# Kernel tuning notes

Hardware: AMD Instinct MI355X
Metric: run time of the kernel (lower is better)

Reference implementation:

```python
import jax, jax.numpy as jnp
import numpy as np

MIN_ROUGHNESS = 0.08
MAX_ROUGHNESS = 0.5
N_MIPS = 6  # 512 -> 16 cubemap mip chain


def _safe_normalize(x, eps=1e-20):
    return x * jax.lax.rsqrt(jnp.clip(jnp.sum(x * x, -1, keepdims=True), eps, None))


def _dot(a, b):
    return jnp.sum(a * b, -1, keepdims=True)


def _cube_face_uv(d):
    # nvdiffrast cube addressing (matches util.cube_to_dir face layout)
    x, y, z = d[..., 0], d[..., 1], d[..., 2]
    ax, ay, az = jnp.abs(x), jnp.abs(y), jnp.abs(z)
    is_x = (ax >= ay) & (ax >= az)
    is_y = (~is_x) & (ay >= az)
    face = jnp.where(is_x, jnp.where(x >= 0, 0, 1),
           jnp.where(is_y, jnp.where(y >= 0, 2, 3), jnp.where(z >= 0, 4, 5)))
    ma = jnp.maximum(jnp.where(is_x, ax, jnp.where(is_y, ay, az)), 1e-20)
    u = jnp.where(face == 0, -z, jnp.where(face == 1, z, jnp.where(face == 5, -x, x))) / ma
    v = jnp.where(face == 2, z, jnp.where(face == 3, -z, -y)) / ma
    return face, u, v


def _bilinear_cube(tex, face, u, v):
    # tex: [6,R,R,C]; face/u/v: [...]; edge-clamped bilinear within the face
    R = tex.shape[1]
    tu = (u * 0.5 + 0.5) * R - 0.5
    tv = (v * 0.5 + 0.5) * R - 0.5
    x0 = jnp.floor(tu); y0 = jnp.floor(tv)
    fx = (tu - x0)[..., None]; fy = (tv - y0)[..., None]
    x0i = jnp.clip(x0, 0, R - 1).astype(jnp.int32)
    x1i = jnp.clip(x0 + 1, 0, R - 1).astype(jnp.int32)
    y0i = jnp.clip(y0, 0, R - 1).astype(jnp.int32)
    y1i = jnp.clip(y0 + 1, 0, R - 1).astype(jnp.int32)
    c00 = tex[face, y0i, x0i]; c01 = tex[face, y0i, x1i]
    c10 = tex[face, y1i, x0i]; c11 = tex[face, y1i, x1i]
    return (c00 * (1 - fx) + c01 * fx) * (1 - fy) + (c10 * (1 - fx) + c11 * fx) * fy


def _sample_cubemap(tex, dirs):
    f, u, v = _cube_face_uv(dirs)
    return _bilinear_cube(tex, f, u, v)


def _sample_2d_clamp(tex, uv):
    # tex: [H,W,C]; uv in [0,1]^2, clamp boundary bilinear (FG LUT lookup)
    H, W = tex.shape[0], tex.shape[1]
    tu = uv[..., 0] * W - 0.5
    tv = uv[..., 1] * H - 0.5
    x0 = jnp.floor(tu); y0 = jnp.floor(tv)
    fx = (tu - x0)[..., None]; fy = (tv - y0)[..., None]
    x0i = jnp.clip(x0, 0, W - 1).astype(jnp.int32)
    x1i = jnp.clip(x0 + 1, 0, W - 1).astype(jnp.int32)
    y0i = jnp.clip(y0, 0, H - 1).astype(jnp.int32)
    y1i = jnp.clip(y0 + 1, 0, H - 1).astype(jnp.int32)
    c00 = tex[y0i, x0i]; c01 = tex[y0i, x1i]
    c10 = tex[y1i, x0i]; c11 = tex[y1i, x1i]
    return (c00 * (1 - fx) + c01 * fx) * (1 - fy) + (c10 * (1 - fx) + c11 * fx) * fy


def _get_mip(r, n_levels):
    lo = (jnp.clip(r, MIN_ROUGHNESS, MAX_ROUGHNESS) - MIN_ROUGHNESS) / (MAX_ROUGHNESS - MIN_ROUGHNESS) * (n_levels - 2)
    hi = (jnp.clip(r, MAX_ROUGHNESS, 1.0) - MAX_ROUGHNESS) / (1.0 - MAX_ROUGHNESS) + (n_levels - 2)
    return jnp.where(r < MAX_ROUGHNESS, lo, hi)


def _linear2srgb(x):
    xs = jnp.where(x > 0.0031308, x, 1.0)  # avoid pow(0) grad issues
    return jnp.where(x > 0.0031308, 1.055 * jnp.power(xs, 1.0 / 2.4) - 0.055, 12.92 * x)


def _avg_pool_cube(c):
    F, R, _, C = c.shape
    return c.reshape(F, R // 2, 2, R // 2, 2, C).mean(axis=(2, 4))


def setup_inputs() -> dict:
    key = jax.random.key(0)
    ks = jax.random.split(key, 10)
    B, H, W = 1, 1024, 1024
    gb_pos = jax.random.normal(ks[0], (B, H, W, 3), jnp.float32)
    gb_normal = _safe_normalize(jax.random.normal(ks[1], (B, H, W, 3), jnp.float32))
    basecolor = jax.random.uniform(ks[2], (B, H, W, 3), jnp.float32)
    metallic = jax.random.uniform(ks[3], (B, H, W, 1), jnp.float32)
    roughness = jax.random.uniform(ks[4], (B, H, W, 1), jnp.float32)
    view_pos = jax.random.normal(ks[5], (1, 1, 1, 3), jnp.float32) * 3.0
    diffuse = jax.random.uniform(ks[6], (6, 16, 16, 3), jnp.float32)
    fg_lut = jax.random.uniform(ks[7], (256, 256, 2), jnp.float32)
    specs = {}
    s = jax.random.uniform(ks[8], (6, 512, 512, 3), jnp.float32)
    for l in range(N_MIPS):
        specs['spec%d' % l] = s
        if l < N_MIPS - 1:
            s = _avg_pool_cube(s)
    return dict(gb_pos=gb_pos, gb_normal=gb_normal, basecolor=basecolor,
                metallic=metallic, roughness=roughness, view_pos=view_pos,
                diffuse=diffuse, fg_lut=fg_lut, **specs)


def reference(gb_pos, gb_normal, basecolor, metallic, roughness, view_pos,
              diffuse, fg_lut, spec0, spec1, spec2, spec3, spec4, spec5):
    specs = [spec0, spec1, spec2, spec3, spec4, spec5]
    L = len(specs)
    metallic = metallic[..., :1]
    wo = _safe_normalize(view_pos - gb_pos)
    diffuse_albedo = (1.0 - metallic) * basecolor
    specular_albedo = 0.04 * (1.0 - metallic) + metallic * basecolor
    reflvec = _safe_normalize(2.0 * _dot(wo, gb_normal) * gb_normal - wo)
    # diffuse IBL: cubemap gather along normal
    ambient = _sample_cubemap(diffuse, gb_normal)
    diffuse_linear = ambient * diffuse_albedo
    # FG LUT gather
    NdotV = jnp.clip(_dot(wo, gb_normal), 1e-4, None)
    fg = _sample_2d_clamp(fg_lut, jnp.concatenate([NdotV, roughness], -1))
    # trilinear (linear-mipmap-linear) specular cubemap gather
    mip = jnp.clip(_get_mip(roughness[..., 0], L), 0.0, L - 1.0)
    face, u, v = _cube_face_uv(reflvec)
    spec = jnp.zeros(gb_pos.shape[:-1] + (spec0.shape[-1],), gb_pos.dtype)
    for l in range(L):
        w = jnp.clip(1.0 - jnp.abs(mip - l), 0.0, 1.0)[..., None]
        spec = spec + w * _bilinear_cube(specs[l], face, u, v)
    reflectance = specular_albedo * fg[..., 0:1] + fg[..., 1:2]
    rgb = spec * reflectance + diffuse_linear
    return _linear2srgb(jnp.clip(rgb, 0.0, 1.0))
```

## Files before the change

### kernel.cpp

```cpp
#include <hip/hip_runtime.h>
#include <hip/hip_fp16.h>

struct V3 { float x, y, z; };

__device__ __forceinline__ V3 v3add(V3 a, V3 b){ return {a.x+b.x, a.y+b.y, a.z+b.z}; }
__device__ __forceinline__ V3 v3sub(V3 a, V3 b){ return {a.x-b.x, a.y-b.y, a.z-b.z}; }
__device__ __forceinline__ V3 v3scale(V3 a, float s){ return {a.x*s, a.y*s, a.z*s}; }
__device__ __forceinline__ V3 v3mul(V3 a, V3 b){ return {a.x*b.x, a.y*b.y, a.z*b.z}; }
__device__ __forceinline__ float dot3(V3 a, V3 b){ return fmaf(a.x,b.x, fmaf(a.y,b.y, a.z*b.z)); }
__device__ __forceinline__ V3 nrm3(V3 a){
    float s = rsqrtf(fmaxf(dot3(a,a), 1e-20f));
    return v3scale(a, s);
}

#define OFF0 0
#define OFF1 1572864
#define OFF2 1966080
#define OFF3 2064384
#define OFF4 2088960
#define OFF5 2095104
#define DIFF_OFF 2096640
#define SPEC_DIFF_COUNT 2098176

struct __align__(16) PairBlock { __half2 h01, h23, h45, h67; };
#define FG_OFF 2098176
#define TOTAL_BLOCKS 2163712
#define PACK_ONLY_BLOCKS 2098176
#define WS_BYTES_FULL  ((size_t)TOTAL_BLOCKS * 16)
#define WS_BYTES_PACK  ((size_t)PACK_ONLY_BLOCKS * 16)

#define Q10_FG_COUNT 65536
#define Q10_COUNT (SPEC_DIFF_COUNT + Q10_FG_COUNT)
#define APP_DIFF 0
#define APP_M5   1536
#define APP_UINTS 3072
#define WS_BYTES_Q10M ((size_t)Q10_COUNT * 16 + (size_t)APP_UINTS * 4)

__device__ __forceinline__ void cube_face_uv(V3 d, int& face, float& u, float& v){
    float ax = fabsf(d.x), ay = fabsf(d.y), az = fabsf(d.z);
    bool is_x = (ax >= ay) && (ax >= az);
    bool is_y = (!is_x) && (ay >= az);
    face = is_x ? (d.x >= 0.f ? 0 : 1)
                : (is_y ? (d.y >= 0.f ? 2 : 3)
                        : (d.z >= 0.f ? 4 : 5));
    float ma = fmaxf(is_x ? ax : (is_y ? ay : az), 1e-20f);
    float un = (face == 0) ? -d.z : (face == 1) ? d.z : (face == 5) ? -d.x : d.x;
    float vn = (face == 2) ?  d.z : (face == 3) ? -d.z : -d.y;
    float inv = 1.0f / ma;
    u = un * inv;
    v = vn * inv;
}

__device__ __forceinline__ void quad_coord_cube(float u, float v, int R,
                                                int& xq, int& yq, float& fx, float& fy){
    float Rf = (float)R;
    float tu = fmaf(fmaf(u, 0.5f, 0.5f), Rf, -0.5f);
    float tv = fmaf(fmaf(v, 0.5f, 0.5f), Rf, -0.5f);
    float x0f = floorf(tu), y0f = floorf(tv);
    fx = tu - x0f; fy = tv - y0f;
    int x0 = (int)x0f, y0 = (int)y0f;
    fx = (x0 < 0) ? 0.f : fx;
    fy = (y0 < 0) ? 0.f : fy;
    xq = min(max(x0, 0), R-1);
    yq = min(max(y0, 0), R-1);
}

__device__ __forceinline__ void quad_coord_2d(float u, float v, int W, int H,
                                              int& xq, int& yq, float& fx, float& fy){
    float tu = fmaf(u, (float)W, -0.5f);
    float tv = fmaf(v, (float)H, -0.5f);
    float x0f = floorf(tu), y0f = floorf(tv);
    fx = tu - x0f; fy = tv - y0f;
    int x0 = (int)x0f, y0 = (int)y0f;
    fx = (x0 < 0) ? 0.f : fx;
    fy = (y0 < 0) ? 0.f : fy;
    xq = min(max(x0, 0), W-1);
    yq = min(max(y0, 0), H-1);
}

__device__ __forceinline__ V3 q10_blend(uint4 q, float fx, float fy){
    float w00 = (1.f-fx)*(1.f-fy), w01 = fx*(1.f-fy);
    float w10 = (1.f-fx)*fy,       w11 = fx*fy;
    float r = (float)(q.x & 1023u)*w00 + (float)(q.y & 1023u)*w01
            + (float)(q.z & 1023u)*w10 + (float)(q.w & 1023u)*w11;
    float g = (float)((q.x>>10) & 1023u)*w00 + (float)((q.y>>10) & 1023u)*w01
            + (float)((q.z>>10) & 1023u)*w10 + (float)((q.w>>10) & 1023u)*w11;
    float b = (float)((q.x>>20) & 1023u)*w00 + (float)((q.y>>20) & 1023u)*w01
            + (float)((q.z>>20) & 1023u)*w10 + (float)((q.w>>20) & 1023u)*w11;
    const float s = 1.0f/1023.0f;
    return { r*s, g*s, b*s };
}

__device__ __forceinline__ void q10_fg(uint4 q, float fx, float fy,
                                       float& fa, float& fb){
    float w00 = (1.f-fx)*(1.f-fy), w01 = fx*(1.f-fy);
    float w10 = (1.f-fx)*fy,       w11 = fx*fy;
    float a00 = (float)(q.x & 1023u),        b00 = (float)((q.x>>10) & 1023u);
    float a01 = (float)((q.x>>20) & 1023u),  b01 = (float)(q.y & 1023u);
    float a10 = (float)((q.y>>10) & 1023u),  b10 = (float)((q.y>>20) & 1023u);
    float a11 = (float)(q.z & 1023u),        b11 = (float)((q.z>>10) & 1023u);
    const float s = 1.0f/1023.0f;
    fa = (a00*w00 + a01*w01 + a10*w10 + a11*w11) * s;
    fb = (b00*w00 + b01*w01 + b10*w10 + b11*w11) * s;
}

__device__ __forceinline__ V3 lds_bilin(const unsigned* lds, int base, int R,
                                        int face, float u, float v){
    float Rf = (float)R;
    float tu = fmaf(fmaf(u, 0.5f, 0.5f), Rf, -0.5f);
    float tv = fmaf(fmaf(v, 0.5f, 0.5f), Rf, -0.5f);
    float x0f = floorf(tu), y0f = floorf(tv);
    float fx = tu - x0f, fy = tv - y0f;
    int x0 = min(max((int)x0f,     0), R-1);
    int x1 = min(max((int)x0f + 1, 0), R-1);
    int y0 = min(max((int)y0f,     0), R-1);
    int y1 = min(max((int)y0f + 1, 0), R-1);
    const unsigned* fb = lds + base + face * R * R;
    uint4 q = make_uint4(fb[y0*R + x0], fb[y0*R + x1],
                         fb[y1*R + x0], fb[y1*R + x1]);
    return q10_blend(q, fx, fy);
}

__device__ __forceinline__ void pair_extract(const PairBlock& pb, V3& lo, V3& hi){
    lo.x = __low2float(pb.h01);  lo.y = __high2float(pb.h01); lo.z = __low2float(pb.h23);
    hi.x = __high2float(pb.h23); hi.y = __low2float(pb.h45);  hi.z = __high2float(pb.h45);
}

__device__ __forceinline__ V3 bilinear_pairtex(const PairBlock* __restrict__ lvl, int R,
                                               int face, float u, float v){
    float Rf = (float)R;
    float tu = fmaf(fmaf(u, 0.5f, 0.5f), Rf, -0.5f);
    float tv = fmaf(fmaf(v, 0.5f, 0.5f), Rf, -0.5f);
    float x0f = floorf(tu), y0f = floorf(tv);
    float fx = tu - x0f,    fy = tv - y0f;
    int x0 = (int)x0f;
    fx = (x0 < 0) ? 0.f : fx;
    int xb  = min(max(x0, 0), R-1);
    int y0i = min(max((int)y0f,     0), R-1);
    int y1i = min(max((int)y0f + 1, 0), R-1);
    const PairBlock* fb = lvl + (size_t)face * R * R;
    PairBlock b0 = fb[(size_t)y0i * R + xb];
    PairBlock b1 = fb[(size_t)y1i * R + xb];
    V3 l0, h0, l1, h1;
    pair_extract(b0, l0, h0);
    pair_extract(b1, l1, h1);
    V3 r0 = { l0.x + (h0.x-l0.x)*fx, l0.y + (h0.y-l0.y)*fx, l0.z + (h0.z-l0.z)*fx };
    V3 r1 = { l1.x + (h1.x-l1.x)*fx, l1.y + (h1.y-l1.y)*fx, l1.z + (h1.z-l1.z)*fx };
    return { r0.x + (r1.x-r0.x)*fy, r0.y + (r1.y-r0.y)*fy, r0.z + (r1.z-r0.z)*fy };
}

__device__ __forceinline__ void sample_fg_pair(const float4* __restrict__ fgp,
                                               float u, float v, float& fa, float& fb){
    const int W = 256, H = 256;
    float tu = fmaf(u, (float)W, -0.5f);
    float tv = fmaf(v, (float)H, -0.5f);
    float x0f = floorf(tu), y0f = floorf(tv);
    float fx = tu - x0f,    fy = tv - y0f;
    int x0 = (int)x0f;
    fx = (x0 < 0) ? 0.f : fx;
    int xb  = min(max(x0, 0), W-1);
    int y0i = min(max((int)y0f,     0), H-1);
    int y1i = min(max((int)y0f + 1, 0), H-1);
    float4 r0 = fgp[(size_t)y0i * W + xb];
    float4 r1 = fgp[(size_t)y1i * W + xb];
    float t0a = r0.x + (r0.z - r0.x)*fx, t0b = r0.y + (r0.w - r0.y)*fx;
    float t1a = r1.x + (r1.z - r1.x)*fx, t1b = r1.y + (r1.w - r1.y)*fx;
    fa = t0a + (t1a - t0a)*fy;
    fb = t0b + (t1b - t0b)*fy;
}

__device__ __forceinline__ V3 bilinear_cube3(const float* __restrict__ tex, int R,
                                             int face, float u, float v){
    float Rf = (float)R;
    float tu = fmaf(fmaf(u, 0.5f, 0.5f), Rf, -0.5f);
    float tv = fmaf(fmaf(v, 0.5f, 0.5f), Rf, -0.5f);
    float x0 = floorf(tu), y0 = floorf(tv);
    float fx = tu - x0,    fy = tv - y0;
    int x0i = min(max((int)x0,     0), R-1);
    int x1i = min(max((int)x0 + 1, 0), R-1);
    int y0i = min(max((int)y0,     0), R-1);
    int y1i = min(max((int)y0 + 1, 0), R-1);
    const float* base = tex + (size_t)face * R * R * 3;
    const float* r0 = base + (size_t)y0i * R * 3;
    const float* r1 = base + (size_t)y1i * R * 3;
    float a0 = r0[3*x0i], a1 = r0[3*x0i+1], a2 = r0[3*x0i+2];
    float b0 = r0[3*x1i], b1 = r0[3*x1i+1], b2 = r0[3*x1i+2];
    float d0 = r1[3*x0i], d1 = r1[3*x0i+1], d2 = r1[3*x0i+2];
    float e0 = r1[3*x1i], e1 = r1[3*x1i+1], e2 = r1[3*x1i+2];
    float w00 = (1.f-fx)*(1.f-fy), w01 = fx*(1.f-fy);
    float w10 = (1.f-fx)*fy,       w11 = fx*fy;
    V3 out;
    out.x = a0*w00 + b0*w01 + d0*w10 + e0*w11;
    out.y = a1*w00 + b1*w01 + d1*w10 + e1*w11;
    out.z = a2*w00 + b2*w01 + d2*w10 + e2*w11;
    return out;
}

__device__ __forceinline__ void sample_fg(const float* __restrict__ lut,
                                          float u, float v, float& fa, float& fb){
    const int W = 256, H = 256;
    float tu = fmaf(u, (float)W, -0.5f);
    float tv = fmaf(v, (float)H, -0.5f);
    float x0 = floorf(tu), y0 = floorf(tv);
    float fx = tu - x0,    fy = tv - y0;
    int x0i = min(max((int)x0,     0), W-1);
    int x1i = min(max((int)x0 + 1, 0), W-1);
    int y0i = min(max((int)y0,     0), H-1);
    int y1i = min(max((int)y0 + 1, 0), H-1);
    const float2* l2 = (const float2*)lut;
    float2 a = l2[(size_t)y0i*W + x0i];
    float2 b = l2[(size_t)y0i*W + x1i];
    float2 d = l2[(size_t)y1i*W + x0i];
    float2 e = l2[(size_t)y1i*W + x1i];
    float w00 = (1.f-fx)*(1.f-fy), w01 = fx*(1.f-fy);
    float w10 = (1.f-fx)*fy,       w11 = fx*fy;
    fa = a.x*w00 + b.x*w01 + d.x*w10 + e.x*w11;
    fb = a.y*w00 + b.y*w01 + d.y*w10 + e.y*w11;
}

__device__ __forceinline__ float lin2srgb(float x){
    float xs = (x > 0.0031308f) ? x : 1.0f;
    float p  = __builtin_amdgcn_exp2f(__builtin_amdgcn_logf(xs) * (1.0f/2.4f));
    return (x > 0.0031308f) ? fmaf(1.055f, p, -0.055f) : 12.92f * x;
}

__device__ __forceinline__ float clamp01(float x){ return fminf(fmaxf(x, 0.f), 1.f); }

struct PixPre {
    V3 diff_alb, spec_alb;
    int sface; float su, sv;
    int dface; float du, dv;
    int offA, RA, offB, RB; float f;
    float ndotv, rough;
};

__device__ __forceinline__ PixPre pre_pixel(
    int i,
    const float* __restrict__ gb_pos, const float* __restrict__ gb_normal,
    const float* __restrict__ basecolor, const float* __restrict__ metallic,
    const float* __restrict__ roughness, V3 vp)
{
    V3 pos = { gb_pos[3*i],    gb_pos[3*i+1],    gb_pos[3*i+2] };
    V3 nrm = { gb_normal[3*i], gb_normal[3*i+1], gb_normal[3*i+2] };
    V3 bc  = { basecolor[3*i], basecolor[3*i+1], basecolor[3*i+2] };
    float m = metallic[i];
    float r = roughness[i];

    V3 wo = nrm3(v3sub(vp, pos));
    float ndv_raw = dot3(wo, nrm);
    V3 refl = nrm3(v3sub(v3scale(nrm, 2.0f*ndv_raw), wo));

    PixPre p;
    float one_m = 1.0f - m;
    p.diff_alb = v3scale(bc, one_m);
    p.spec_alb = { fmaf(m, bc.x, 0.04f*one_m),
                   fmaf(m, bc.y, 0.04f*one_m),
                   fmaf(m, bc.z, 0.04f*one_m) };
    p.ndotv = fmaxf(ndv_raw, 0.0001f);
    p.rough = r;

    const float MIN_R = 0.08f, MAX_R = 0.5f;
    float lo = (fminf(fmaxf(r, MIN_R), MAX_R) - MIN_R) / (MAX_R - MIN_R) * 4.0f;
    float hi = (fminf(fmaxf(r, MAX_R), 1.0f) - MAX_R) / (1.0f - MAX_R) + 4.0f;
    float mip = (r < MAX_R) ? lo : hi;
    mip = fminf(fmaxf(mip, 0.0f), 5.0f);
    int l0 = min((int)mip, 5);
    p.f = mip - (float)l0;
    int l1 = min(l0 + 1, 5);

    int offA = OFF0;
    offA = (l0 == 1) ? OFF1 : offA; offA = (l0 == 2) ? OFF2 : offA;
    offA = (l0 == 3) ? OFF3 : offA; offA = (l0 == 4) ? OFF4 : offA;
    offA = (l0 == 5) ? OFF5 : offA;
    int offB = OFF0;
    offB = (l1 == 1) ? OFF1 : offB; offB = (l1 == 2) ? OFF2 : offB;
    offB = (l1 == 3) ? OFF3 : offB; offB = (l1 == 4) ? OFF4 : offB;
    offB = (l1 == 5) ? OFF5 : offB;
    p.offA = offA; p.RA = 512 >> l0;
    p.offB = offB; p.RB = 512 >> l1;

    cube_face_uv(nrm, p.dface, p.du, p.dv);
    cube_face_uv(refl, p.sface, p.su, p.sv);
    return p;
}

__device__ __forceinline__ unsigned pk3(float a, float b, float c){
    unsigned ia = __float2uint_rn(fminf(fmaxf(a, 0.f), 1.f) * 1023.f);
    unsigned ib = __float2uint_rn(fminf(fmaxf(b, 0.f), 1.f) * 1023.f);
    unsigned ic = __float2uint_rn(fminf(fmaxf(c, 0.f), 1.f) * 1023.f);
    return ia | (ib << 10) | (ic << 20);
}

__global__ __launch_bounds__(256)
void pack_q10m_kernel(const float* __restrict__ s0, const float* __restrict__ s1,
                      const float* __restrict__ s2, const float* __restrict__ s3,
                      const float* __restrict__ s4, const float* __restrict__ s5,
                      const float* __restrict__ diffuse, const float* __restrict__ fg_lut,
                      uint4* __restrict__ qws)
{
    int t = blockIdx.x * blockDim.x + threadIdx.x;
    if (t >= Q10_COUNT + APP_UINTS) return;
    if (t >= Q10_COUNT) {
        int local = t - Q10_COUNT;
        const float* src; int idx;
        if (local < APP_M5) { src = diffuse; idx = local; }
        else                { src = s5;      idx = local - APP_M5; }
        ((unsigned*)(qws + Q10_COUNT))[local] = pk3(src[3*idx], src[3*idx+1], src[3*idx+2]);
        return;
    }
    if (t >= SPEC_DIFF_COUNT) {
        int local = t - SPEC_DIFF_COUNT;
        int x = local & 255, y = local >> 8;
        int i00 = local;
        int i01 = (x == 255) ? local : local + 1;
        int i10 = (y == 255) ? local : local + 256;
        int i11 = (x == 255) ? i10 : i10 + 1;
        uint4 q;
        q.x = pk3(fg_lut[2*i00], fg_lut[2*i00+1], fg_lut[2*i01]);
        q.y = pk3(fg_lut[2*i01+1], fg_lut[2*i10], fg_lut[2*i10+1]);
        q.z = pk3(fg_lut[2*i11], fg_lut[2*i11+1], 0.f);
        q.w = 0u;
        qws[t] = q;
        return;
    }
    const float* src; int local; int Rm, Rsh;
    if      (t >= DIFF_OFF) { src = diffuse; local = t - DIFF_OFF; Rm = 15;  Rsh = 4; }
    else if (t >= OFF5)     { src = s5;      local = t - OFF5;     Rm = 15;  Rsh = 4; }
    else if (t >= OFF4)     { src = s4;      local = t - OFF4;     Rm = 31;  Rsh = 5; }
    else if (t >= OFF3)     { src = s3;      local = t - OFF3;     Rm = 63;  Rsh = 6; }
    else if (t >= OFF2)     { src = s2;      local = t - OFF2;     Rm = 127; Rsh = 7; }
    else if (t >= OFF1)     { src = s1;      local = t - OFF1;     Rm = 255; Rsh = 8; }
    else                    { src = s0;      local = t;            Rm = 511; Rsh = 9; }
    int x = local & Rm;
    int y = (local >> Rsh) & Rm;
    int i00 = local;
    int i01 = (x == Rm) ? local : local + 1;
    int i10 = (y == Rm) ? local : local + (Rm + 1);
    int i11 = (x == Rm) ? i10 : i10 + 1;
    uint4 q;
    q.x = pk3(src[3*i00], src[3*i00+1], src[3*i00+2]);
    q.y = pk3(src[3*i01], src[3*i01+1], src[3*i01+2]);
    q.z = pk3(src[3*i10], src[3*i10+1], src[3*i10+2]);
    q.w = pk3(src[3*i11], src[3*i11+1], src[3*i11+2]);
    qws[t] = q;
}

__device__ __forceinline__ V3 sample_spec(const uint4* __restrict__ qws,
                                          const unsigned* lds,
                                          int off, int R, int face, float u, float v){
    if (R == 16)
        return lds_bilin(lds, APP_M5, 16, face, u, v);
    int x, y; float fx, fy;
    quad_coord_cube(u, v, R, x, y, fx, fy);
    size_t q = (size_t)off + (size_t)face * R * R + (size_t)y * R + x;
    return q10_blend(qws[q], fx, fy);
}

__global__ __launch_bounds__(256)
void envlight_q10m(const float* __restrict__ gb_pos,
                   const float* __restrict__ gb_normal,
                   const float* __restrict__ basecolor,
                   const float* __restrict__ metallic,
                   const float* __restrict__ roughness,
                   const float* __restrict__ view_pos,
                   const uint4* __restrict__ qws,
                   float* __restrict__ out,
                   int n)
{
    __shared__ unsigned lds_small[APP_UINTS];
    {
        const uint4* app4 = qws + Q10_COUNT;
        uint4* l4 = (uint4*)lds_small;
        for (int k = threadIdx.x; k < APP_UINTS/4; k += 256)
            l4[k] = app4[k];
    }
    __syncthreads();

    int i = blockIdx.x * blockDim.x + threadIdx.x;
    if (i >= n) return;
    V3 vp = { view_pos[0], view_pos[1], view_pos[2] };
    PixPre p = pre_pixel(i, gb_pos, gb_normal, basecolor, metallic, roughness, vp);

    int fx_, fy_; float ffx, ffy;
    quad_coord_2d(p.ndotv, p.rough, 256, 256, fx_, fy_, ffx, ffy);
    uint4 F = qws[(size_t)SPEC_DIFF_COUNT + (size_t)fy_ * 256 + fx_];

    V3 specA = sample_spec(qws, lds_small, p.offA, p.RA, p.sface, p.su, p.sv);
    V3 specB = sample_spec(qws, lds_small, p.offB, p.RB, p.sface, p.su, p.sv);
    V3 ambient = lds_bilin(lds_small, APP_DIFF, 16, p.dface, p.du, p.dv);

    float fa, fb;
    q10_fg(F, ffx, ffy, fa, fb);

    V3 spec = { specA.x + (specB.x - specA.x) * p.f,
                specA.y + (specB.y - specA.y) * p.f,
                specA.z + (specB.z - specA.z) * p.f };
    V3 reflc = { fmaf(p.spec_alb.x, fa, fb),
                 fmaf(p.spec_alb.y, fa, fb),
                 fmaf(p.spec_alb.z, fa, fb) };
    V3 rgb = v3add(v3mul(spec, reflc), v3mul(ambient, p.diff_alb));

    out[3*i+0] = lin2srgb(clamp01(rgb.x));
    out[3*i+1] = lin2srgb(clamp01(rgb.y));
    out[3*i+2] = lin2srgb(clamp01(rgb.z));
}

__global__ __launch_bounds__(256)
void pack_kernel(const float* __restrict__ s0, const float* __restrict__ s1,
                 const float* __restrict__ s2, const float* __restrict__ s3,
                 const float* __restrict__ s4, const float* __restrict__ s5,
                 const float* __restrict__ diffuse, const float* __restrict__ fg_lut,
                 PairBlock* __restrict__ ws, int total)
{
    int t = blockIdx.x * blockDim.x + threadIdx.x;
    if (t >= total) return;
    if (t >= FG_OFF) {
        int local = t - FG_OFF;
        int x = local & 255;
        int nb = (x == 255) ? local : local + 1;
        float4 v = make_float4(fg_lut[2*local], fg_lut[2*local+1],
                               fg_lut[2*nb],    fg_lut[2*nb+1]);
        ((float4*)ws)[t] = v;
        return;
    }
    const float* src; int local; int Rmask;
    if      (t >= DIFF_OFF) { src = diffuse; local = t - DIFF_OFF; Rmask = 15;  }
    else if (t >= OFF5)     { src = s5;      local = t - OFF5;     Rmask = 15;  }
    else if (t >= OFF4)     { src = s4;      local = t - OFF4;     Rmask = 31;  }
    else if (t >= OFF3)     { src = s3;      local = t - OFF3;     Rmask = 63;  }
    else if (t >= OFF2)     { src = s2;      local = t - OFF2;     Rmask = 127; }
    else if (t >= OFF1)     { src = s1;      local = t - OFF1;     Rmask = 255; }
    else                    { src = s0;      local = t;            Rmask = 511; }
    int nb = ((local & Rmask) == Rmask) ? local : local + 1;
    float ar = src[3*local], ag = src[3*local+1], ab = src[3*local+2];
    float br = src[3*nb],    bg = src[3*nb+1],    bb = src[3*nb+2];
    PairBlock pb;
    pb.h01 = __floats2half2_rn(ar, ag);
    pb.h23 = __floats2half2_rn(ab, br);
    pb.h45 = __floats2half2_rn(bg, bb);
    pb.h67 = __floats2half2_rn(0.f, 0.f);
    ws[t] = pb;
}

template <bool FGPAIR>
__global__ __launch_bounds__(256)
void envlight_pair(const float* __restrict__ gb_pos,
                   const float* __restrict__ gb_normal,
                   const float* __restrict__ basecolor,
                   const float* __restrict__ metallic,
                   const float* __restrict__ roughness,
                   const float* __restrict__ view_pos,
                   const float* __restrict__ fg_lut,
                   const PairBlock* __restrict__ ws,
                   float* __restrict__ out,
                   int n)
{
    int i = blockIdx.x * blockDim.x + threadIdx.x;
    if (i >= n) return;
    V3 vp = { view_pos[0], view_pos[1], view_pos[2] };
    PixPre p = pre_pixel(i, gb_pos, gb_normal, basecolor, metallic, roughness, vp);
    V3 specA   = bilinear_pairtex(ws + p.offA, p.RA, p.sface, p.su, p.sv);
    V3 specB   = bilinear_pairtex(ws + p.offB, p.RB, p.sface, p.su, p.sv);
    V3 ambient = bilinear_pairtex(ws + DIFF_OFF, 16, p.dface, p.du, p.dv);
    float fa, fb;
    if (FGPAIR) sample_fg_pair((const float4*)(ws + FG_OFF), p.ndotv, p.rough, fa, fb);
    else        sample_fg(fg_lut, p.ndotv, p.rough, fa, fb);
    V3 spec = { specA.x + (specB.x - specA.x) * p.f,
                specA.y + (specB.y - specA.y) * p.f,
                specA.z + (specB.z - specA.z) * p.f };
    V3 reflc = { fmaf(p.spec_alb.x, fa, fb),
                 fmaf(p.spec_alb.y, fa, fb),
                 fmaf(p.spec_alb.z, fa, fb) };
    V3 rgb = v3add(v3mul(spec, reflc), v3mul(ambient, p.diff_alb));
    out[3*i+0] = lin2srgb(clamp01(rgb.x));
    out[3*i+1] = lin2srgb(clamp01(rgb.y));
    out[3*i+2] = lin2srgb(clamp01(rgb.z));
}

__global__ __launch_bounds__(256)
void envlight_fallback(const float* __restrict__ gb_pos,
                       const float* __restrict__ gb_normal,
                       const float* __restrict__ basecolor,
                       const float* __restrict__ metallic,
                       const float* __restrict__ roughness,
                       const float* __restrict__ view_pos,
                       const float* __restrict__ diffuse,
                       const float* __restrict__ fg_lut,
                       const float* __restrict__ s0, const float* __restrict__ s1,
                       const float* __restrict__ s2, const float* __restrict__ s3,
                       const float* __restrict__ s4, const float* __restrict__ s5,
                       float* __restrict__ out, int n)
{
    int i = blockIdx.x * blockDim.x + threadIdx.x;
    if (i >= n) return;
    V3 vp = { view_pos[0], view_pos[1], view_pos[2] };
    PixPre p = pre_pixel(i, gb_pos, gb_normal, basecolor, metallic, roughness, vp);
    int l0 = 0;
    l0 = (p.offA == OFF1) ? 1 : l0; l0 = (p.offA == OFF2) ? 2 : l0;
    l0 = (p.offA == OFF3) ? 3 : l0; l0 = (p.offA == OFF4) ? 4 : l0;
    l0 = (p.offA == OFF5) ? 5 : l0;
    int l1 = 0;
    l1 = (p.offB == OFF1) ? 1 : l1; l1 = (p.offB == OFF2) ? 2 : l1;
    l1 = (p.offB == OFF3) ? 3 : l1; l1 = (p.offB == OFF4) ? 4 : l1;
    l1 = (p.offB == OFF5) ? 5 : l1;
    const float* tA = s0;
    tA = (l0 == 1) ? s1 : tA; tA = (l0 == 2) ? s2 : tA;
    tA = (l0 == 3) ? s3 : tA; tA = (l0 == 4) ? s4 : tA; tA = (l0 == 5) ? s5 : tA;
    const float* tB = s0;
    tB = (l1 == 1) ? s1 : tB; tB = (l1 == 2) ? s2 : tB;
    tB = (l1 == 3) ? s3 : tB; tB = (l1 == 4) ? s4 : tB; tB = (l1 == 5) ? s5 : tB;
    V3 ambient = bilinear_cube3(diffuse, 16, p.dface, p.du, p.dv);
    V3 specA   = bilinear_cube3(tA, p.RA, p.sface, p.su, p.sv);
    V3 specB   = bilinear_cube3(tB, p.RB, p.sface, p.su, p.sv);
    float fa, fb;
    sample_fg(fg_lut, p.ndotv, p.rough, fa, fb);
    V3 spec = { specA.x + (specB.x - specA.x) * p.f,
                specA.y + (specB.y - specA.y) * p.f,
                specA.z + (specB.z - specA.z) * p.f };
    V3 reflc = { fmaf(p.spec_alb.x, fa, fb),
                 fmaf(p.spec_alb.y, fa, fb),
                 fmaf(p.spec_alb.z, fa, fb) };
    V3 rgb = v3add(v3mul(spec, reflc), v3mul(ambient, p.diff_alb));
    out[3*i+0] = lin2srgb(clamp01(rgb.x));
    out[3*i+1] = lin2srgb(clamp01(rgb.y));
    out[3*i+2] = lin2srgb(clamp01(rgb.z));
}

extern "C" void kernel_launch(void* const* d_in, const int* in_sizes, int n_in,
                              void* d_out, int out_size, void* d_ws, size_t ws_size,
                              hipStream_t stream) {
    const float* gb_pos    = (const float*)d_in[0];
    const float* gb_normal = (const float*)d_in[1];
    const float* basecolor = (const float*)d_in[2];
    const float* metallic  = (const float*)d_in[3];
    const float* roughness = (const float*)d_in[4];
    const float* view_pos  = (const float*)d_in[5];
    const float* diffuse   = (const float*)d_in[6];
    const float* fg_lut    = (const float*)d_in[7];
    const float* s0        = (const float*)d_in[8];
    const float* s1        = (const float*)d_in[9];
    const float* s2        = (const float*)d_in[10];
    const float* s3        = (const float*)d_in[11];
    const float* s4        = (const float*)d_in[12];
    const float* s5        = (const float*)d_in[13];
    float* out = (float*)d_out;

    int n = in_sizes[0] / 3;
    int block = 256;
    int grid = (n + block - 1) / block;

    if (ws_size >= WS_BYTES_Q10M) {
        uint4* qws = (uint4*)d_ws;
        int ptotal = Q10_COUNT + APP_UINTS;
        int pgrid = (ptotal + block - 1) / block;
        pack_q10m_kernel<<<pgrid, block, 0, stream>>>(s0, s1, s2, s3, s4, s5,
                                                      diffuse, fg_lut, qws);
        envlight_q10m<<<grid, block, 0, stream>>>(gb_pos, gb_normal, basecolor,
            metallic, roughness, view_pos, qws, out, n);
    } else if (ws_size >= WS_BYTES_PACK) {
        bool full = ws_size >= WS_BYTES_FULL;
        PairBlock* ws = (PairBlock*)d_ws;
        int total = full ? TOTAL_BLOCKS : PACK_ONLY_BLOCKS;
        int pgrid = (total + block - 1) / block;
        pack_kernel<<<pgrid, block, 0, stream>>>(s0, s1, s2, s3, s4, s5,
                                                 diffuse, fg_lut, ws, total);
        if (full)
            envlight_pair<true><<<grid, block, 0, stream>>>(gb_pos, gb_normal,
                basecolor, metallic, roughness, view_pos, fg_lut, ws, out, n);
        else
            envlight_pair<false><<<grid, block, 0, stream>>>(gb_pos, gb_normal,
                basecolor, metallic, roughness, view_pos, fg_lut, ws, out, n);
    } else {
        envlight_fallback<<<grid, block, 0, stream>>>(gb_pos, gb_normal, basecolor,
            metallic, roughness, view_pos, diffuse, fg_lut,
            s0, s1, s2, s3, s4, s5, out, n);
    }
}
```

Measured before the change: 152.4 us.

## Vectorize pack and shading kernels to process four texels/pixels per thread

The pack kernel now handles four packed quad-texels per thread, reading source rows with float4 loads and reusing the packed neighbors, so each source value is loaded and quantized once rather than four times. The shading kernel processes four pixels per thread with float4 loads and stores on the AoS inputs and output. This cuts redundant global loads and scalar 4-byte accesses. In exchange there are 4x fewer threads, which lowers occupancy and latency hiding for the gather-heavy shading, and register pressure goes up.

```diff
diff --git a/kernel.cpp b/kernel.cpp
--- a/kernel.cpp
+++ b/kernel.cpp
@@ -35,6 +35,11 @@
 #define APP_M5   1536
 #define APP_UINTS 3072
 #define WS_BYTES_Q10M ((size_t)Q10_COUNT * 16 + (size_t)APP_UINTS * 4)
+
+#define Q4_SPEC (SPEC_DIFF_COUNT/4)
+#define Q4_FG   (Q10_FG_COUNT/4)
+#define Q4_APP  (APP_UINTS/4)
+#define Q4_TOTAL (Q4_SPEC + Q4_FG + Q4_APP)
 
 __device__ __forceinline__ void cube_face_uv(V3 d, int& face, float& u, float& v){
     float ax = fabsf(d.x), ay = fabsf(d.y), az = fabsf(d.z);
@@ -234,18 +239,8 @@
     float ndotv, rough;
 };
 
-__device__ __forceinline__ PixPre pre_pixel(
-    int i,
-    const float* __restrict__ gb_pos, const float* __restrict__ gb_normal,
-    const float* __restrict__ basecolor, const float* __restrict__ metallic,
-    const float* __restrict__ roughness, V3 vp)
-{
-    V3 pos = { gb_pos[3*i],    gb_pos[3*i+1],    gb_pos[3*i+2] };
-    V3 nrm = { gb_normal[3*i], gb_normal[3*i+1], gb_normal[3*i+2] };
-    V3 bc  = { basecolor[3*i], basecolor[3*i+1], basecolor[3*i+2] };
-    float m = metallic[i];
-    float r = roughness[i];
-
+__device__ __forceinline__ PixPre pre_pixel_v(V3 pos, V3 nrm, V3 bc, float m, float r, V3 vp)
+{
     V3 wo = nrm3(v3sub(vp, pos));
     float ndv_raw = dot3(wo, nrm);
     V3 refl = nrm3(v3sub(v3scale(nrm, 2.0f*ndv_raw), wo));
@@ -284,6 +279,18 @@
     return p;
 }
 
+__device__ __forceinline__ PixPre pre_pixel(
+    int i,
+    const float* __restrict__ gb_pos, const float* __restrict__ gb_normal,
+    const float* __restrict__ basecolor, const float* __restrict__ metallic,
+    const float* __restrict__ roughness, V3 vp)
+{
+    V3 pos = { gb_pos[3*i],    gb_pos[3*i+1],    gb_pos[3*i+2] };
+    V3 nrm = { gb_normal[3*i], gb_normal[3*i+1], gb_normal[3*i+2] };
+    V3 bc  = { basecolor[3*i], basecolor[3*i+1], basecolor[3*i+2] };
+    return pre_pixel_v(pos, nrm, bc, metallic[i], roughness[i], vp);
+}
+
 __device__ __forceinline__ unsigned pk3(float a, float b, float c){
     unsigned ia = __float2uint_rn(fminf(fmaxf(a, 0.f), 1.f) * 1023.f);
     unsigned ib = __float2uint_rn(fminf(fmaxf(b, 0.f), 1.f) * 1023.f);
@@ -292,57 +299,100 @@
 }
 
 __global__ __launch_bounds__(256)
-void pack_q10m_kernel(const float* __restrict__ s0, const float* __restrict__ s1,
-                      const float* __restrict__ s2, const float* __restrict__ s3,
-                      const float* __restrict__ s4, const float* __restrict__ s5,
-                      const float* __restrict__ diffuse, const float* __restrict__ fg_lut,
-                      uint4* __restrict__ qws)
+void pack_q10m_v4(const float* __restrict__ s0, const float* __restrict__ s1,
+                  const float* __restrict__ s2, const float* __restrict__ s3,
+                  const float* __restrict__ s4, const float* __restrict__ s5,
+                  const float* __restrict__ diffuse, const float* __restrict__ fg_lut,
+                  uint4* __restrict__ qws)
 {
     int t = blockIdx.x * blockDim.x + threadIdx.x;
-    if (t >= Q10_COUNT + APP_UINTS) return;
-    if (t >= Q10_COUNT) {
-        int local = t - Q10_COUNT;
+    if (t >= Q4_TOTAL) return;
+
+    if (t >= Q4_SPEC + Q4_FG) {
+        int local4 = (t - Q4_SPEC - Q4_FG) * 4;
         const float* src; int idx;
-        if (local < APP_M5) { src = diffuse; idx = local; }
-        else                { src = s5;      idx = local - APP_M5; }
-        ((unsigned*)(qws + Q10_COUNT))[local] = pk3(src[3*idx], src[3*idx+1], src[3*idx+2]);
+        if (local4 < APP_M5) { src = diffuse; idx = local4; }
+        else                 { src = s5;      idx = local4 - APP_M5; }
+        const float4* sp = (const float4*)(src + 3*idx);
+        float4 a = sp[0], b = sp[1], c = sp[2];
+        uint4 o;
+        o.x = pk3(a.x, a.y, a.z);
+        o.y = pk3(a.w, b.x, b.y);
+        o.z = pk3(b.z, b.w, c.x);
+        o.w = pk3(c.y, c.z, c.w);
+        *(uint4*)((unsigned*)(qws + Q10_COUNT) + local4) = o;
         return;
     }
-    if (t >= SPEC_DIFF_COUNT) {
-        int local = t - SPEC_DIFF_COUNT;
+
+    if (t >= Q4_SPEC) {
+        int local = (t - Q4_SPEC) * 4;
         int x = local & 255, y = local >> 8;
-        int i00 = local;
-        int i01 = (x == 255) ? local : local + 1;
-        int i10 = (y == 255) ? local : local + 256;
-        int i11 = (x == 255) ? i10 : i10 + 1;
-        uint4 q;
-        q.x = pk3(fg_lut[2*i00], fg_lut[2*i00+1], fg_lut[2*i01]);
-        q.y = pk3(fg_lut[2*i01+1], fg_lut[2*i10], fg_lut[2*i10+1]);
-        q.z = pk3(fg_lut[2*i11], fg_lut[2*i11+1], 0.f);
-        q.w = 0u;
-        qws[t] = q;
+        int y1 = (y == 255) ? y : y + 1;
+        const float* r0p = fg_lut + 2*local;
+        const float* r1p = fg_lut + 2*((y1 << 8) + x);
+        bool edge = (x == 252);
+        float4 r0a = ((const float4*)r0p)[0], r0b = ((const float4*)r0p)[1];
+        float4 r1a = ((const float4*)r1p)[0], r1b = ((const float4*)r1p)[1];
+        float4 r0c = *(const float4*)(r0p + (edge ? 4 : 8));
+        float4 r1c = *(const float4*)(r1p + (edge ? 4 : 8));
+        float a0[5], b0[5], a1[5], b1[5];
+        a0[0]=r0a.x; b0[0]=r0a.y; a0[1]=r0a.z; b0[1]=r0a.w;
+        a0[2]=r0b.x; b0[2]=r0b.y; a0[3]=r0b.z; b0[3]=r0b.w;
+        a0[4]= edge ? r0b.z : r0c.x; b0[4]= edge ? r0b.w : r0c.y;
+        a1[0]=r1a.x; b1[0]=r1a.y; a1[1]=r1a.z; b1[1]=r1a.w;
+        a1[2]=r1b.x; b1[2]=r1b.y; a1[3]=r1b.z; b1[3]=r1b.w;
+        a1[4]= edge ? r1b.z : r1c.x; b1[4]= edge ? r1b.w : r1c.y;
+        #pragma unroll
+        for (int k = 0; k < 4; ++k) {
+            uint4 q;
+            q.x = pk3(a0[k], b0[k], a0[k+1]);
+            q.y = pk3(b0[k+1], a1[k], b1[k]);
+            q.z = pk3(a1[k+1], b1[k+1], 0.f);
+            q.w = 0u;
+            qws[(size_t)SPEC_DIFF_COUNT + local + k] = q;
+        }
         return;
     }
-    const float* src; int local; int Rm, Rsh;
-    if      (t >= DIFF_OFF) { src = diffuse; local = t - DIFF_OFF; Rm = 15;  Rsh = 4; }
-    else if (t >= OFF5)     { src = s5;      local = t - OFF5;     Rm = 15;  Rsh = 4; }
-    else if (t >= OFF4)     { src = s4;      local = t - OFF4;     Rm = 31;  Rsh = 5; }
-    else if (t >= OFF3)     { src = s3;      local = t - OFF3;     Rm = 63;  Rsh = 6; }
-    else if (t >= OFF2)     { src = s2;      local = t - OFF2;     Rm = 127; Rsh = 7; }
-    else if (t >= OFF1)     { src = s1;      local = t - OFF1;     Rm = 255; Rsh = 8; }
-    else                    { src = s0;      local = t;            Rm = 511; Rsh = 9; }
+
+    int local4q = t * 4;
+    const float* src; int local; int Rm;
+    if      (local4q >= DIFF_OFF) { src = diffuse; local = local4q - DIFF_OFF; Rm = 15;  }
+    else if (local4q >= OFF5)     { src = s5;      local = local4q - OFF5;     Rm = 15;  }
+    else if (local4q >= OFF4)     { src = s4;      local = local4q - OFF4;     Rm = 31;  }
+    else if (local4q >= OFF3)     { src = s3;      local = local4q - OFF3;     Rm = 63;  }
+    else if (local4q >= OFF2)     { src = s2;      local = local4q - OFF2;     Rm = 127; }
+    else if (local4q >= OFF1)     { src = s1;      local = local4q - OFF1;     Rm = 255; }
+    else                          { src = s0;      local = local4q;            Rm = 511; }
     int x = local & Rm;
-    int y = (local >> Rsh) & Rm;
-    int i00 = local;
-    int i01 = (x == Rm) ? local : local + 1;
-    int i10 = (y == Rm) ? local : local + (Rm + 1);
-    int i11 = (x == Rm) ? i10 : i10 + 1;
-    uint4 q;
-    q.x = pk3(src[3*i00], src[3*i00+1], src[3*i00+2]);
-    q.y = pk3(src[3*i01], src[3*i01+1], src[3*i01+2]);
-    q.z = pk3(src[3*i10], src[3*i10+1], src[3*i10+2]);
-    q.w = pk3(src[3*i11], src[3*i11+1], src[3*i11+2]);
-    qws[t] = q;
+    int y = (local / (Rm + 1)) & Rm;
+    int rowUp = (y == Rm) ? 0 : (Rm + 1);
+    const float* r0p = src + 3*local;
+    const float* r1p = src + 3*(local + rowUp);
+    bool edge = (x + 4 > Rm);
+    float4 A0 = ((const float4*)r0p)[0], A1 = ((const float4*)r0p)[1], A2 = ((const float4*)r0p)[2];
+    float4 B0 = ((const float4*)r1p)[0], B1 = ((const float4*)r1p)[1], B2 = ((const float4*)r1p)[2];
+    float4 A3 = *(const float4*)(r0p + (edge ? 8 : 12));
+    float4 B3 = *(const float4*)(r1p + (edge ? 8 : 12));
+    unsigned t0[5], t1[5];
+    t0[0] = pk3(A0.x, A0.y, A0.z);
+    t0[1] = pk3(A0.w, A1.x, A1.y);
+    t0[2] = pk3(A1.z, A1.w, A2.x);
+    t0[3] = pk3(A2.y, A2.z, A2.w);
+    t0[4] = edge ? t0[3] : pk3(A3.x, A3.y, A3.z);
+    t1[0] = pk3(B0.x, B0.y, B0.z);
+    t1[1] = pk3(B0.w, B1.x, B1.y);
+    t1[2] = pk3(B1.z, B1.w, B2.x);
+    t1[3] = pk3(B2.y, B2.z, B2.w);
+    t1[4] = edge ? t1[3] : pk3(B3.x, B3.y, B3.z);
+    #pragma unroll
+    for (int k = 0; k < 4; ++k) {
+        uint4 q;
+        q.x = t0[k];
+        q.y = t0[k+1];
+        q.z = t1[k];
+        q.w = t1[k+1];
+        qws[(size_t)local4q + k] = q;
+    }
 }
 
 __device__ __forceinline__ V3 sample_spec(const uint4* __restrict__ qws,
@@ -356,16 +406,46 @@
     return q10_blend(qws[q], fx, fy);
 }
 
+__device__ __forceinline__ void shade_px(V3 pos, V3 nrm, V3 bc, float m, float r, V3 vp,
+                                         const uint4* __restrict__ qws,
+                                         const unsigned* lds, float* o)
+{
+    PixPre p = pre_pixel_v(pos, nrm, bc, m, r, vp);
+
+    int fx_, fy_; float ffx, ffy;
+    quad_coord_2d(p.ndotv, p.rough, 256, 256, fx_, fy_, ffx, ffy);
+    uint4 F = qws[(size_t)SPEC_DIFF_COUNT + (size_t)fy_ * 256 + fx_];
+
+    V3 specA = sample_spec(qws, lds, p.offA, p.RA, p.sface, p.su, p.sv);
+    V3 specB = sample_spec(qws, lds, p.offB, p.RB, p.sface, p.su, p.sv);
+    V3 ambient = lds_bilin(lds, APP_DIFF, 16, p.dface, p.du, p.dv);
+
+    float fa, fb;
+    q10_fg(F, ffx, ffy, fa, fb);
+
+    V3 spec = { specA.x + (specB.x - specA.x) * p.f,
+                specA.y + (specB.y - specA.y) * p.f,
+                specA.z + (specB.z - specA.z) * p.f };
+    V3 reflc = { fmaf(p.spec_alb.x, fa, fb),
+                 fmaf(p.spec_alb.y, fa, fb),
+                 fmaf(p.spec_alb.z, fa, fb) };
+    V3 rgb = v3add(v3mul(spec, reflc), v3mul(ambient, p.diff_alb));
+
+    o[0] = lin2srgb(clamp01(rgb.x));
+    o[1] = lin2srgb(clamp01(rgb.y));
+    o[2] = lin2srgb(clamp01(rgb.z));
+}
+
 __global__ __launch_bounds__(256)
-void envlight_q10m(const float* __restrict__ gb_pos,
-                   const float* __restrict__ gb_normal,
-                   const float* __restrict__ basecolor,
-                   const float* __restrict__ metallic,
-                   const float* __restrict__ roughness,
-                   const float* __restrict__ view_pos,
-                   const uint4* __restrict__ qws,
-                   float* __restrict__ out,
-                   int n)
+void envlight_q10m_v4(const float* __restrict__ gb_pos,
+                      const float* __restrict__ gb_normal,
+                      const float* __restrict__ basecolor,
+                      const float* __restrict__ metallic,
+                      const float* __restrict__ roughness,
+                      const float* __restrict__ view_pos,
+                      const uint4* __restrict__ qws,
+                      float* __restrict__ out,
+                      int n)
 {
     __shared__ unsigned lds_small[APP_UINTS];
     {
@@ -376,33 +456,52 @@
     }
     __syncthreads();
 
-    int i = blockIdx.x * blockDim.x + threadIdx.x;
-    if (i >= n) return;
+    int t = blockIdx.x * blockDim.x + threadIdx.x;
+    int i0 = t * 4;
+    if (i0 >= n) return;
     V3 vp = { view_pos[0], view_pos[1], view_pos[2] };
-    PixPre p = pre_pixel(i, gb_pos, gb_normal, basecolor, metallic, roughness, vp);
-
-    int fx_, fy_; float ffx, ffy;
-    quad_coord_2d(p.ndotv, p.rough, 256, 256, fx_, fy_, ffx, ffy);
-    uint4 F = qws[(size_t)SPEC_DIFF_COUNT + (size_t)fy_ * 256 + fx_];
-
-    V3 specA = sample_spec(qws, lds_small, p.offA, p.RA, p.sface, p.su, p.sv);
-    V3 specB = sample_spec(qws, lds_small, p.offB, p.RB, p.sface, p.su, p.sv);
-    V3 ambient = lds_bilin(lds_small, APP_DIFF, 16, p.dface, p.du, p.dv);
-
-    float fa, fb;
-    q10_fg(F, ffx, ffy, fa, fb);
-
-    V3 spec = { specA.x + (specB.x - specA.x) * p.f,
-                specA.y + (specB.y - specA.y) * p.f,
-                specA.z + (specB.z - specA.z) * p.f };
-    V3 reflc = { fmaf(p.spec_alb.x, fa, fb),
-                 fmaf(p.spec_alb.y, fa, fb),
-                 fmaf(p.spec_alb.z, fa, fb) };
-    V3 rgb = v3add(v3mul(spec, reflc), v3mul(ambient, p.diff_alb));
-
-    out[3*i+0] = lin2srgb(clamp01(rgb.x));
-    out[3*i+1] = lin2srgb(clamp01(rgb.y));
-    out[3*i+2] = lin2srgb(clamp01(rgb.z));
+
+    if (i0 + 3 < n) {
+        const float4* P = (const float4*)(gb_pos    + 3*i0);
+        const float4* N = (const float4*)(gb_normal + 3*i0);
+        const float4* B = (const float4*)(basecolor + 3*i0);
+        float4 p0 = P[0], p1 = P[1], p2 = P[2];
+        float4 n0 = N[0], n1 = N[1], n2 = N[2];
+        float4 b0 = B[0], b1 = B[1], b2 = B[2];
+        float4 mt = *(const float4*)(metallic  + i0);
+        float4 rg = *(const float4*)(roughness + i0);
+
+        float pf[12] = { p0.x,p0.y,p0.z,p0.w, p1.x,p1.y,p1.z,p1.w, p2.x,p2.y,p2.z,p2.w };
+        float nf[12] = { n0.x,n0.y,n0.z,n0.w, n1.x,n1.y,n1.z,n1.w, n2.x,n2.y,n2.z,n2.w };
+        float bf[12] = { b0.x,b0.y,b0.z,b0.w, b1.x,b1.y,b1.z,b1.w, b2.x,b2.y,b2.z,b2.w };
+        float mf[4]  = { mt.x, mt.y, mt.z, mt.w };
+        float rf[4]  = { rg.x, rg.y, rg.z, rg.w };
+        float of[12];
+
+        #pragma unroll
+        for (int j = 0; j < 4; ++j) {
+            V3 pos = { pf[3*j], pf[3*j+1], pf[3*j+2] };
+            V3 nrm = { nf[3*j], nf[3*j+1], nf[3*j+2] };
+            V3 bc  = { bf[3*j], bf[3*j+1], bf[3*j+2] };
+            shade_px(pos, nrm, bc, mf[j], rf[j], vp, qws, lds_small, of + 3*j);
+        }
+
+        float4* O = (float4*)(out + 3*i0);
+        O[0] = make_float4(of[0], of[1], of[2],  of[3]);
+        O[1] = make_float4(of[4], of[5], of[6],  of[7]);
+        O[2] = make_float4(of[8], of[9], of[10], of[11]);
+    } else {
+        for (int j = 0; j < 4; ++j) {
+            int i = i0 + j;
+            if (i >= n) break;
+            V3 pos = { gb_pos[3*i],    gb_pos[3*i+1],    gb_pos[3*i+2] };
+            V3 nrm = { gb_normal[3*i], gb_normal[3*i+1], gb_normal[3*i+2] };
+            V3 bc  = { basecolor[3*i], basecolor[3*i+1], basecolor[3*i+2] };
+            float o[3];
+            shade_px(pos, nrm, bc, metallic[i], roughness[i], vp, qws, lds_small, o);
+            out[3*i+0] = o[0]; out[3*i+1] = o[1]; out[3*i+2] = o[2];
+        }
+    }
 }
 
 __global__ __launch_bounds__(256)
@@ -551,11 +650,12 @@
 
     if (ws_size >= WS_BYTES_Q10M) {
         uint4* qws = (uint4*)d_ws;
-        int ptotal = Q10_COUNT + APP_UINTS;
-        int pgrid = (ptotal + block - 1) / block;
-        pack_q10m_kernel<<<pgrid, block, 0, stream>>>(s0, s1, s2, s3, s4, s5,
-                                                      diffuse, fg_lut, qws);
-        envlight_q10m<<<grid, block, 0, stream>>>(gb_pos, gb_normal, basecolor,
+        int pgrid = (Q4_TOTAL + block - 1) / block;
+        pack_q10m_v4<<<pgrid, block, 0, stream>>>(s0, s1, s2, s3, s4, s5,
+                                                  diffuse, fg_lut, qws);
+        int t4 = (n + 3) / 4;
+        int mgrid = (t4 + block - 1) / block;
+        envlight_q10m_v4<<<mgrid, block, 0, stream>>>(gb_pos, gb_normal, basecolor,
             metallic, roughness, view_pos, qws, out, n);
     } else if (ws_size >= WS_BYTES_PACK) {
         bool full = ws_size >= WS_BYTES_FULL;
```

After: 155.8 us. +2.2%, slower.
